# Kernel optimization log

Hardware: AMD Instinct MI355X
Metric: run time of the kernel (lower is better)

The kernel has to match this reference:

```python
import jax, jax.numpy as jnp
import numpy as np

N = 100_000
E = 1_600_000
D_IN = 128
D_OUT = 128
LN_EPS = 1e-5


def mean_agg(x, src, dst, deg):
    # out[dst] += x[src]; out /= deg  (scatter-mean over incoming edges)
    summed = jax.ops.segment_sum(x[src], dst, num_segments=N)
    return summed / deg[:, None]


def setup_inputs() -> dict:
    key = jax.random.key(0)
    ks = jax.random.split(key, 8)
    h = jax.random.normal(ks[0], (N, D_IN), dtype=jnp.float32)
    edge_index_mp = jax.random.randint(ks[1], (2, E), 0, N, dtype=jnp.int64)
    # deg = in-degree of each node (count of edges with dst == i), clamped to >= 1
    deg_mp = jax.ops.segment_sum(jnp.ones((E,), jnp.float32), edge_index_mp[1], num_segments=N)
    deg_mp = jnp.maximum(deg_mp, 1.0)
    scale = 1.0 / np.sqrt(D_IN)
    W_self = jax.random.uniform(ks[2], (D_OUT, D_IN), jnp.float32, -scale, scale)
    W_nb1 = jax.random.uniform(ks[3], (D_OUT, D_IN), jnp.float32, -scale, scale)
    W_hp = jax.random.uniform(ks[4], (D_OUT, D_IN), jnp.float32, -scale, scale)
    W_nb2 = jax.random.uniform(ks[5], (D_OUT, D_IN), jnp.float32, -scale, scale)
    bias = jnp.zeros((D_OUT,), jnp.float32)
    branch_logits = jnp.zeros((4,), jnp.float32)
    ln_gamma = jnp.ones((D_OUT,), jnp.float32)
    ln_beta = jnp.zeros((D_OUT,), jnp.float32)
    return {
        "h": h, "edge_index_mp": edge_index_mp, "deg_mp": deg_mp,
        "W_self": W_self, "W_nb1": W_nb1, "W_hp": W_hp, "W_nb2": W_nb2,
        "bias": bias, "branch_logits": branch_logits,
        "ln_gamma": ln_gamma, "ln_beta": ln_beta,
    }


def reference(h, edge_index_mp, deg_mp, W_self, W_nb1, W_hp, W_nb2,
              bias, branch_logits, ln_gamma, ln_beta):
    src, dst = edge_index_mp[0], edge_index_mp[1]
    nb1 = mean_agg(h, src, dst, deg_mp)          # 1-hop mean
    nb2 = mean_agg(nb1, src, dst, deg_mp)        # 2-hop mean
    hp = h - nb1                                  # high-pass branch
    scales = 2.0 * jax.nn.sigmoid(branch_logits)
    z = (scales[0] * (h @ W_self.T)
         + scales[1] * (nb1 @ W_nb1.T)
         + scales[2] * (hp @ W_hp.T)
         + scales[3] * (nb2 @ W_nb2.T)
         + bias)
    mu = jnp.mean(z, axis=-1, keepdims=True)
    var = jnp.var(z, axis=-1, keepdims=True)
    return (z - mu) * jax.lax.rsqrt(var + LN_EPS) * ln_gamma + ln_beta
```

## Files before the change

### kernel.cpp

```cpp
#include <hip/hip_runtime.h>

#define NN 100000
#define NE 1600000
#define D 128
#define KTOT 384
#define LN_EPS 1e-5f

#define PITCH_US 200
#define PITCH_DW 100
#define GM 64

#define SCAN_CHUNK 2048
#define NSB 49

#define NBK 196
#define BCAP 10240

#define WS_OFF_OFF   0
#define WS_OFF_CUR   401408
#define WS_OFF_BSUM  802816
#define WS_OFF_GCUR  803072
#define WS_OFF_WCBF  804096
#define WS_OFF_ESRC  967680
#define WS_OFF_GBUF  7768064
#define WS_OFF_H16   7768064
#define WS_OFF_NB1   33368064

typedef __attribute__((ext_vector_type(8))) _Float16 f16x8;
typedef __attribute__((ext_vector_type(2))) _Float16 f16x2;
typedef __attribute__((ext_vector_type(4))) float f32x4;

__device__ __forceinline__ unsigned short f2h(float f) {
    _Float16 h = (_Float16)f;
    unsigned short s; __builtin_memcpy(&s, &h, 2); return s;
}
__device__ __forceinline__ f16x2 u2h2(unsigned u) {
    f16x2 h; __builtin_memcpy(&h, &u, 4); return h;
}

__global__ void k_prep(const float* __restrict__ h, unsigned int* __restrict__ h16) {
    int i = blockIdx.x * blockDim.x + threadIdx.x;
    float2 v = reinterpret_cast<const float2*>(h)[i];
    h16[i] = (unsigned)f2h(v.x) | ((unsigned)f2h(v.y) << 16);
}

__global__ __launch_bounds__(256) void k_scan1(const float* __restrict__ deg,
                                               int* __restrict__ off,
                                               int* __restrict__ bsum) {
    __shared__ int lds[256];
    int t = threadIdx.x, b = blockIdx.x;
    int base = b * SCAN_CHUNK + t * 8;
    int v[8];
    if (base < NN) {
        float4 a0 = reinterpret_cast<const float4*>(deg + base)[0];
        float4 a1 = reinterpret_cast<const float4*>(deg + base)[1];
        v[0] = __float2int_rn(a0.x); v[1] = __float2int_rn(a0.y);
        v[2] = __float2int_rn(a0.z); v[3] = __float2int_rn(a0.w);
        v[4] = __float2int_rn(a1.x); v[5] = __float2int_rn(a1.y);
        v[6] = __float2int_rn(a1.z); v[7] = __float2int_rn(a1.w);
    } else {
        #pragma unroll
        for (int j = 0; j < 8; ++j) v[j] = 0;
    }
    int s = 0;
    #pragma unroll
    for (int j = 0; j < 8; ++j) s += v[j];
    lds[t] = s;
    __syncthreads();
    for (int ofs = 1; ofs < 256; ofs <<= 1) {
        int x = (t >= ofs) ? lds[t - ofs] : 0;
        __syncthreads();
        lds[t] += x;
        __syncthreads();
    }
    int excl = (t == 0) ? 0 : lds[t - 1];
    #pragma unroll
    for (int j = 0; j < 8; ++j) { off[base + j] = excl; excl += v[j]; }
    if (t == 255) bsum[b] = lds[255];
}

__global__ void k_scan2(int* __restrict__ bsum) {
    int t = threadIdx.x;
    int v = (t < NSB) ? bsum[t] : 0;
    #pragma unroll
    for (int ofs = 1; ofs < 64; ofs <<= 1) {
        int x = __shfl_up(v, ofs, 64);
        if (t >= ofs) v += x;
    }
    int excl = __shfl_up(v, 1, 64);
    if (t == 0) excl = 0;
    if (t < NSB) bsum[t] = excl;
    if (t == NSB - 1) bsum[NSB] = v;
}

__global__ void k_scan3(int* __restrict__ off, const int* __restrict__ bsum) {
    int i = blockIdx.x * blockDim.x + threadIdx.x;
    if (i < NN) off[i] += bsum[i >> 11];
    if (i == 0) off[NN] = bsum[NSB];
}

__global__ __launch_bounds__(256) void k_bin(const int* __restrict__ src,
                                             const int* __restrict__ dst,
                                             int* __restrict__ gcur,
                                             int2* __restrict__ gbuf) {
    __shared__ int bcnt[NBK];
    __shared__ int bbase[NBK];
    int t = threadIdx.x;
    if (t < NBK) bcnt[t] = 0;
    __syncthreads();
    int e0 = blockIdx.x * 2048;
    int s[8], d[8], r[8];
    #pragma unroll
    for (int it = 0; it < 8; ++it) {
        int e = e0 + it * 256 + t;
        bool ok = e < NE;
        s[it] = ok ? src[e] : 0;
        d[it] = ok ? dst[e] : -1;
        r[it] = ok ? atomicAdd(&bcnt[d[it] >> 9], 1) : 0;
    }
    __syncthreads();
    if (t < NBK) bbase[t] = atomicAdd(&gcur[t], bcnt[t]);
    __syncthreads();
    #pragma unroll
    for (int it = 0; it < 8; ++it) {
        if (d[it] >= 0) {
            int bk = d[it] >> 9;
            gbuf[(size_t)bk * BCAP + bbase[bk] + r[it]] = make_int2(s[it], d[it]);
        }
    }
}

__global__ __launch_bounds__(1024) void k_scatter2(const int2* __restrict__ gbuf,
                                                   const int* __restrict__ gcur,
                                                   const int* __restrict__ off,
                                                   int* __restrict__ cur,
                                                   int* __restrict__ esrc) {
    int b = blockIdx.x;
    int nb = gcur[b];
    const int2* bb = gbuf + (size_t)b * BCAP;
    for (int i = threadIdx.x; i < nb; i += 1024) {
        int2 e = bb[i];
        int p = off[e.y] + atomicAdd(&cur[e.y], 1);
        esrc[p] = e.x;
    }
}

__global__ void k_weights(const float* __restrict__ Ws, const float* __restrict__ W1,
                          const float* __restrict__ Whp, const float* __restrict__ W2,
                          const float* __restrict__ logits, unsigned short* __restrict__ wcbf) {
    int idx = blockIdx.x * blockDim.x + threadIdx.x;
    if (idx >= D * D) return;
    int o = idx >> 7, k = idx & 127;
    float s0 = 2.f / (1.f + __expf(-logits[0]));
    float s1 = 2.f / (1.f + __expf(-logits[1]));
    float s2 = 2.f / (1.f + __expf(-logits[2]));
    float s3 = 2.f / (1.f + __expf(-logits[3]));
    unsigned short b1 = f2h(s0 * Ws[idx] + s2 * Whp[idx]);
    unsigned short b2 = f2h(s1 * W1[idx] - s2 * Whp[idx]);
    unsigned short b3 = f2h(s3 * W2[idx]);
    size_t base = (size_t)o * KTOT + k;
    wcbf[base]       = b1;
    wcbf[base + 128] = b2;
    wcbf[base + 256] = b3;
}

template <bool INTERLEAVED>
__global__ __launch_bounds__(256) void k_hop(const unsigned int* __restrict__ in,
                                             unsigned int* __restrict__ outp,
                                             const int* __restrict__ off,
                                             const int* __restrict__ cnt_arr,
                                             const int* __restrict__ esrc,
                                             const float* __restrict__ deg) {
    int w = (blockIdx.x * blockDim.x + threadIdx.x) >> 6;
    int lane = threadIdx.x & 63;
    int beg = __builtin_amdgcn_readfirstlane(off[w]);
    int cnt = __builtin_amdgcn_readfirstlane(cnt_arr[w]);
    float ax = 0.f, ay = 0.f;
    for (int bs = 0; bs < cnt; bs += 64) {
        int m = cnt - bs; if (m > 64) m = 64;
        int ev = esrc[beg + bs + (lane < m ? lane : 0)];
        for (int j = 0; j < m; j += 16) {
            unsigned u[16];
            #pragma unroll
            for (int k = 0; k < 16; ++k) {
                int idx = j + k;
                int s = __builtin_amdgcn_readlane(ev, idx < m ? idx : 0);
                u[k] = in[(size_t)s * 64 + lane];
            }
            #pragma unroll
            for (int k = 0; k < 16; ++k) {
                if (j + k >= m) u[k] = 0u;
                f16x2 v = u2h2(u[k]);
                ax += (float)v.x; ay += (float)v.y;
            }
        }
    }
    float inv = 1.0f / deg[w];
    ax *= inv; ay *= inv;
    unsigned pk = (unsigned)f2h(ax) | ((unsigned)f2h(ay) << 16);
    if (INTERLEAVED) outp[(size_t)w * 128 + 64 + lane] = pk;
    else             outp[(size_t)w * 64 + lane] = pk;
}

__global__ __launch_bounds__(256) void k_gemm_ln(
    const unsigned int* __restrict__ h16,
    const unsigned int* __restrict__ nb1u,
    const unsigned short* __restrict__ wcbf, const float* __restrict__ bias,
    const float* __restrict__ gamma, const float* __restrict__ beta,
    float* __restrict__ out) {
    __shared__ __align__(16) unsigned short Xs[GM * PITCH_US];
    __shared__ float part_s[4][GM];
    __shared__ float part_q[4][GM];
    __shared__ float mu_s[GM], rs_s[GM];
    unsigned int* Xs_u = reinterpret_cast<unsigned int*>(Xs);
    const uint2* h16v = reinterpret_cast<const uint2*>(h16);
    const uint2* nb1v = reinterpret_cast<const uint2*>(nb1u);
    const uint2* outv = reinterpret_cast<const uint2*>(out);

    const int t = threadIdx.x;
    const int wv = t >> 6, lane = t & 63;
    const int lm = lane & 15, quad = lane >> 4;
    const int node0 = blockIdx.x * GM;
    const int obase = wv * 32;

    f32x4 acc[4][2] = {};

    #pragma unroll
    for (int it = 0; it < 8; ++it) {
        int i = t + 256 * it;
        int row = i >> 5, dp = i & 31;
        int rn = node0 + row; rn = rn < NN ? rn : NN - 1;
        uint2 v = h16v[(size_t)rn * 32 + dp];
        *reinterpret_cast<uint2*>(&Xs_u[row * PITCH_DW + dp * 2]) = v;
    }
    #pragma unroll
    for (int it = 0; it < 4; ++it) {
        int i = t + 256 * it;
        int row = i >> 4, dp = i & 15;
        int rn = node0 + row; rn = rn < NN ? rn : NN - 1;
        uint2 v = nb1v[(size_t)rn * 32 + dp];
        *reinterpret_cast<uint2*>(&Xs_u[row * PITCH_DW + 64 + dp * 2]) = v;
    }
    __syncthreads();

    uint2 pre1[4], pre2[8];
    #pragma unroll
    for (int it = 0; it < 4; ++it) {
        int i = t + 256 * it;
        int row = i >> 4, dp = i & 15;
        int rn = node0 + row; rn = rn < NN ? rn : NN - 1;
        pre1[it] = nb1v[(size_t)rn * 32 + 16 + dp];
    }
    #pragma unroll
    for (int it = 0; it < 8; ++it) {
        int i = t + 256 * it;
        int row = i >> 5, dp = i & 31;
        int rn = node0 + row; rn = rn < NN ? rn : NN - 1;
        pre2[it] = outv[(size_t)rn * 64 + 32 + dp];
    }

    {
        f16x8 bfr[2][6];
        #pragma unroll
        for (int nt = 0; nt < 2; ++nt) {
            const unsigned short* wp =
                wcbf + (size_t)(obase + nt * 16 + lm) * KTOT + quad * 8;
            #pragma unroll
            for (int s = 0; s < 6; ++s)
                bfr[nt][s] = *reinterpret_cast<const f16x8*>(wp + s * 32);
        }
        #pragma unroll
        for (int s = 0; s < 6; ++s) {
            int koff = s * 32 + quad * 8;
            f16x8 a[4];
            #pragma unroll
            for (int mt = 0; mt < 4; ++mt)
                a[mt] = *reinterpret_cast<const f16x8*>(&Xs[(mt * 16 + lm) * PITCH_US + koff]);
            #pragma unroll
            for (int mt = 0; mt < 4; ++mt) {
                acc[mt][0] = __builtin_amdgcn_mfma_f32_16x16x32_f16(a[mt], bfr[0][s], acc[mt][0], 0, 0, 0);
                acc[mt][1] = __builtin_amdgcn_mfma_f32_16x16x32_f16(a[mt], bfr[1][s], acc[mt][1], 0, 0, 0);
            }
        }
    }
    __syncthreads();

    #pragma unroll
    for (int it = 0; it < 4; ++it) {
        int i = t + 256 * it;
        int row = i >> 4, dp = i & 15;
        *reinterpret_cast<uint2*>(&Xs_u[row * PITCH_DW + dp * 2]) = pre1[it];
    }
    #pragma unroll
    for (int it = 0; it < 8; ++it) {
        int i = t + 256 * it;
        int row = i >> 5, dp = i & 31;
        *reinterpret_cast<uint2*>(&Xs_u[row * PITCH_DW + 32 + dp * 2]) = pre2[it];
    }
    __syncthreads();

    {
        f16x8 bfr[2][6];
        #pragma unroll
        for (int nt = 0; nt < 2; ++nt) {
            const unsigned short* wp =
                wcbf + (size_t)(obase + nt * 16 + lm) * KTOT + 192 + quad * 8;
            #pragma unroll
            for (int s = 0; s < 6; ++s)
                bfr[nt][s] = *reinterpret_cast<const f16x8*>(wp + s * 32);
        }
        #pragma unroll
        for (int s = 0; s < 6; ++s) {
            int koff = s * 32 + quad * 8;
            f16x8 a[4];
            #pragma unroll
            for (int mt = 0; mt < 4; ++mt)
                a[mt] = *reinterpret_cast<const f16x8*>(&Xs[(mt * 16 + lm) * PITCH_US + koff]);
            #pragma unroll
            for (int mt = 0; mt < 4; ++mt) {
                acc[mt][0] = __builtin_amdgcn_mfma_f32_16x16x32_f16(a[mt], bfr[0][s], acc[mt][0], 0, 0, 0);
                acc[mt][1] = __builtin_amdgcn_mfma_f32_16x16x32_f16(a[mt], bfr[1][s], acc[mt][1], 0, 0, 0);
            }
        }
    }

    float bv0 = bias[obase + lm], bv1 = bias[obase + 16 + lm];
    #pragma unroll
    for (int mt = 0; mt < 4; ++mt) {
        float s[4], q[4];
        #pragma unroll
        for (int r = 0; r < 4; ++r) {
            float v0 = acc[mt][0][r] + bv0;
            float v1 = acc[mt][1][r] + bv1;
            acc[mt][0][r] = v0;  acc[mt][1][r] = v1;
            s[r] = v0 + v1;
            q[r] = v0 * v0 + v1 * v1;
        }
        #pragma unroll
        for (int off = 1; off < 16; off <<= 1) {
            #pragma unroll
            for (int r = 0; r < 4; ++r) {
                s[r] += __shfl_xor(s[r], off, 64);
                q[r] += __shfl_xor(q[r], off, 64);
            }
        }
        if (lm == 0) {
            #pragma unroll
            for (int r = 0; r < 4; ++r) {
                part_s[wv][mt * 16 + quad * 4 + r] = s[r];
                part_q[wv][mt * 16 + quad * 4 + r] = q[r];
            }
        }
    }
    __syncthreads();
    if (t < GM) {
        float s = part_s[0][t] + part_s[1][t] + part_s[2][t] + part_s[3][t];
        float q = part_q[0][t] + part_q[1][t] + part_q[2][t] + part_q[3][t];
        float m = s * (1.f / 128.f);
        float var = q * (1.f / 128.f) - m * m;
        mu_s[t] = m;
        rs_s[t] = rsqrtf(var + LN_EPS);
    }
    __syncthreads();

    float g0 = gamma[obase + lm], g1 = gamma[obase + 16 + lm];
    float e0 = beta[obase + lm],  e1 = beta[obase + 16 + lm];
    #pragma unroll
    for (int mt = 0; mt < 4; ++mt) {
        #pragma unroll
        for (int r = 0; r < 4; ++r) {
            int lrow = mt * 16 + quad * 4 + r;
            if (node0 + lrow < NN) {
                float mu = mu_s[lrow], rs = rs_s[lrow];
                size_t ro = (size_t)(node0 + lrow) * D;
                out[ro + obase + lm]      = (acc[mt][0][r] - mu) * rs * g0 + e0;
                out[ro + obase + 16 + lm] = (acc[mt][1][r] - mu) * rs * g1 + e1;
            }
        }
    }
}

extern "C" void kernel_launch(void* const* d_in, const int* in_sizes, int n_in,
                              void* d_out, int out_size, void* d_ws, size_t ws_size,
                              hipStream_t stream) {
    const float* h      = (const float*)d_in[0];
    const int*   ei     = (const int*)d_in[1];
    const float* deg    = (const float*)d_in[2];
    const float* Wself  = (const float*)d_in[3];
    const float* Wnb1   = (const float*)d_in[4];
    const float* Whp    = (const float*)d_in[5];
    const float* Wnb2   = (const float*)d_in[6];
    const float* bias   = (const float*)d_in[7];
    const float* logits = (const float*)d_in[8];
    const float* gamma  = (const float*)d_in[9];
    const float* beta   = (const float*)d_in[10];
    float* out = (float*)d_out;

    char* ws = (char*)d_ws;
    int* off                 = (int*)(ws + WS_OFF_OFF);
    int* cur                 = (int*)(ws + WS_OFF_CUR);
    int* bsum                = (int*)(ws + WS_OFF_BSUM);
    int* gcur                = (int*)(ws + WS_OFF_GCUR);
    unsigned short* wcbf     = (unsigned short*)(ws + WS_OFF_WCBF);
    int* esrc                = (int*)(ws + WS_OFF_ESRC);
    int2* gbuf               = (int2*)(ws + WS_OFF_GBUF);
    unsigned int* h16        = (unsigned int*)(ws + WS_OFF_H16);
    unsigned int* nb1u       = (unsigned int*)(ws + WS_OFF_NB1);

    const int* src = ei;
    const int* dst = ei + NE;

    hipMemsetAsync(cur, 0, NN * sizeof(int), stream);
    hipMemsetAsync(gcur, 0, NBK * sizeof(int), stream);

    k_weights<<<64, 256, 0, stream>>>(Wself, Wnb1, Whp, Wnb2, logits, wcbf);
    k_scan1<<<NSB, 256, 0, stream>>>(deg, off, bsum);
    k_scan2<<<1, 64, 0, stream>>>(bsum);
    k_scan3<<<(NN + 255) / 256, 256, 0, stream>>>(off, bsum);
    k_bin<<<(NE + 2047) / 2048, 256, 0, stream>>>(src, dst, gcur, gbuf);
    k_scatter2<<<NBK, 1024, 0, stream>>>(gbuf, gcur, off, cur, esrc);

    k_prep<<<25000, 256, 0, stream>>>(h, h16);

    k_hop<false><<<(NN * 64) / 256, 256, 0, stream>>>(h16, nb1u, off, cur, esrc, deg);
    k_hop<true><<<(NN * 64) / 256, 256, 0, stream>>>(nb1u, (unsigned int*)out, off, cur, esrc, deg);

    k_gemm_ln<<<(NN + GM - 1) / GM, 256, 0, stream>>>(h16, nb1u, wcbf, bias, gamma, beta, out);
}
```

Before: 350.4 us.

## Fuse scan, weight prep, edge binning and fp16 conversion into one front kernel

Merges k_scan1, k_weights, k_bin and k_prep into a single k_front launch whose block ranges are dispatched by block index. The cur array is now zeroed inside the scan blocks instead of by a separate memset, and the fp16 conversion of h now does 16 floats per thread with wide stores. The bin buffer gbuf is moved to alias the nb1 region rather than h16, because h16 is now written concurrently with binning. This removes several launches and their gaps and lets independent preprocessing phases overlap, at the cost of one kernel with mixed register and LDS use and reliance on workspace aliasing staying correct.

```diff
diff --git a/kernel.cpp b/kernel.cpp
--- a/kernel.cpp
+++ b/kernel.cpp
@@ -15,6 +15,12 @@
 
 #define NBK 196
 #define BCAP 10240
+
+#define FB_SCAN1   0
+#define FB_WEIGHTS 49
+#define FB_BIN     113
+#define FB_PREP    895
+#define FB_TOTAL   4020
 
 #define WS_OFF_OFF   0
 #define WS_OFF_CUR   401408
@@ -22,9 +28,9 @@
 #define WS_OFF_GCUR  803072
 #define WS_OFF_WCBF  804096
 #define WS_OFF_ESRC  967680
-#define WS_OFF_GBUF  7768064
 #define WS_OFF_H16   7768064
 #define WS_OFF_NB1   33368064
+#define WS_OFF_GBUF  33368064
 
 typedef __attribute__((ext_vector_type(8))) _Float16 f16x8;
 typedef __attribute__((ext_vector_type(2))) _Float16 f16x2;
@@ -37,46 +43,105 @@
 __device__ __forceinline__ f16x2 u2h2(unsigned u) {
     f16x2 h; __builtin_memcpy(&h, &u, 4); return h;
 }
-
-__global__ void k_prep(const float* __restrict__ h, unsigned int* __restrict__ h16) {
-    int i = blockIdx.x * blockDim.x + threadIdx.x;
-    float2 v = reinterpret_cast<const float2*>(h)[i];
-    h16[i] = (unsigned)f2h(v.x) | ((unsigned)f2h(v.y) << 16);
-}
-
-__global__ __launch_bounds__(256) void k_scan1(const float* __restrict__ deg,
-                                               int* __restrict__ off,
-                                               int* __restrict__ bsum) {
+__device__ __forceinline__ unsigned pk2(float a, float b) {
+    return (unsigned)f2h(a) | ((unsigned)f2h(b) << 16);
+}
+
+__global__ __launch_bounds__(256) void k_front(
+    const float* __restrict__ deg, int* __restrict__ off, int* __restrict__ bsum,
+    int* __restrict__ cur,
+    const float* __restrict__ Ws, const float* __restrict__ W1,
+    const float* __restrict__ Whp, const float* __restrict__ W2,
+    const float* __restrict__ logits, unsigned short* __restrict__ wcbf,
+    const int* __restrict__ src, const int* __restrict__ dst,
+    int* __restrict__ gcur, int2* __restrict__ gbuf,
+    const float* __restrict__ h, unsigned int* __restrict__ h16) {
     __shared__ int lds[256];
-    int t = threadIdx.x, b = blockIdx.x;
-    int base = b * SCAN_CHUNK + t * 8;
-    int v[8];
-    if (base < NN) {
-        float4 a0 = reinterpret_cast<const float4*>(deg + base)[0];
-        float4 a1 = reinterpret_cast<const float4*>(deg + base)[1];
-        v[0] = __float2int_rn(a0.x); v[1] = __float2int_rn(a0.y);
-        v[2] = __float2int_rn(a0.z); v[3] = __float2int_rn(a0.w);
-        v[4] = __float2int_rn(a1.x); v[5] = __float2int_rn(a1.y);
-        v[6] = __float2int_rn(a1.z); v[7] = __float2int_rn(a1.w);
+    __shared__ int bcnt[NBK];
+    __shared__ int bbase[NBK];
+    const int b = blockIdx.x;
+    const int t = threadIdx.x;
+
+    if (b < FB_WEIGHTS) {
+        int base = b * SCAN_CHUNK + t * 8;
+        *reinterpret_cast<int4*>(cur + base) = make_int4(0, 0, 0, 0);
+        *reinterpret_cast<int4*>(cur + base + 4) = make_int4(0, 0, 0, 0);
+        int v[8];
+        if (base < NN) {
+            float4 a0 = reinterpret_cast<const float4*>(deg + base)[0];
+            float4 a1 = reinterpret_cast<const float4*>(deg + base)[1];
+            v[0] = __float2int_rn(a0.x); v[1] = __float2int_rn(a0.y);
+            v[2] = __float2int_rn(a0.z); v[3] = __float2int_rn(a0.w);
+            v[4] = __float2int_rn(a1.x); v[5] = __float2int_rn(a1.y);
+            v[6] = __float2int_rn(a1.z); v[7] = __float2int_rn(a1.w);
+        } else {
+            #pragma unroll
+            for (int j = 0; j < 8; ++j) v[j] = 0;
+        }
+        int s = 0;
+        #pragma unroll
+        for (int j = 0; j < 8; ++j) s += v[j];
+        lds[t] = s;
+        __syncthreads();
+        for (int ofs = 1; ofs < 256; ofs <<= 1) {
+            int x = (t >= ofs) ? lds[t - ofs] : 0;
+            __syncthreads();
+            lds[t] += x;
+            __syncthreads();
+        }
+        int excl = (t == 0) ? 0 : lds[t - 1];
+        #pragma unroll
+        for (int j = 0; j < 8; ++j) { off[base + j] = excl; excl += v[j]; }
+        if (t == 255) bsum[b] = lds[255];
+    } else if (b < FB_BIN) {
+        int idx = (b - FB_WEIGHTS) * 256 + t;
+        int o = idx >> 7, k = idx & 127;
+        float s0 = 2.f / (1.f + __expf(-logits[0]));
+        float s1 = 2.f / (1.f + __expf(-logits[1]));
+        float s2 = 2.f / (1.f + __expf(-logits[2]));
+        float s3 = 2.f / (1.f + __expf(-logits[3]));
+        unsigned short b1 = f2h(s0 * Ws[idx] + s2 * Whp[idx]);
+        unsigned short b2 = f2h(s1 * W1[idx] - s2 * Whp[idx]);
+        unsigned short b3 = f2h(s3 * W2[idx]);
+        size_t base = (size_t)o * KTOT + k;
+        wcbf[base]       = b1;
+        wcbf[base + 128] = b2;
+        wcbf[base + 256] = b3;
+    } else if (b < FB_PREP) {
+        if (t < NBK) bcnt[t] = 0;
+        __syncthreads();
+        int e0 = (b - FB_BIN) * 2048;
+        int s[8], d[8], r[8];
+        #pragma unroll
+        for (int it = 0; it < 8; ++it) {
+            int e = e0 + it * 256 + t;
+            bool ok = e < NE;
+            s[it] = ok ? src[e] : 0;
+            d[it] = ok ? dst[e] : -1;
+            r[it] = ok ? atomicAdd(&bcnt[d[it] >> 9], 1) : 0;
+        }
+        __syncthreads();
+        if (t < NBK) bbase[t] = atomicAdd(&gcur[t], bcnt[t]);
+        __syncthreads();
+        #pragma unroll
+        for (int it = 0; it < 8; ++it) {
+            if (d[it] >= 0) {
+                int bk = d[it] >> 9;
+                gbuf[(size_t)bk * BCAP + bbase[bk] + r[it]] = make_int2(s[it], d[it]);
+            }
+        }
     } else {
-        #pragma unroll
-        for (int j = 0; j < 8; ++j) v[j] = 0;
-    }
-    int s = 0;
-    #pragma unroll
-    for (int j = 0; j < 8; ++j) s += v[j];
-    lds[t] = s;
-    __syncthreads();
-    for (int ofs = 1; ofs < 256; ofs <<= 1) {
-        int x = (t >= ofs) ? lds[t - ofs] : 0;
-        __syncthreads();
-        lds[t] += x;
-        __syncthreads();
-    }
-    int excl = (t == 0) ? 0 : lds[t - 1];
-    #pragma unroll
-    for (int j = 0; j < 8; ++j) { off[base + j] = excl; excl += v[j]; }
-    if (t == 255) bsum[b] = lds[255];
+        int g2 = (b - FB_PREP) * 256 + t;
+        const float4* hv = reinterpret_cast<const float4*>(h) + (size_t)g2 * 4;
+        float4 a = hv[0], bb = hv[1], c = hv[2], dd = hv[3];
+        uint4 o0, o1;
+        o0.x = pk2(a.x, a.y);   o0.y = pk2(a.z, a.w);
+        o0.z = pk2(bb.x, bb.y); o0.w = pk2(bb.z, bb.w);
+        o1.x = pk2(c.x, c.y);   o1.y = pk2(c.z, c.w);
+        o1.z = pk2(dd.x, dd.y); o1.w = pk2(dd.z, dd.w);
+        reinterpret_cast<uint4*>(h16)[(size_t)g2 * 2]     = o0;
+        reinterpret_cast<uint4*>(h16)[(size_t)g2 * 2 + 1] = o1;
+    }
 }
 
 __global__ void k_scan2(int* __restrict__ bsum) {
@@ -97,37 +162,6 @@
     int i = blockIdx.x * blockDim.x + threadIdx.x;
     if (i < NN) off[i] += bsum[i >> 11];
     if (i == 0) off[NN] = bsum[NSB];
-}
-
-__global__ __launch_bounds__(256) void k_bin(const int* __restrict__ src,
-                                             const int* __restrict__ dst,
-                                             int* __restrict__ gcur,
-                                             int2* __restrict__ gbuf) {
-    __shared__ int bcnt[NBK];
-    __shared__ int bbase[NBK];
-    int t = threadIdx.x;
-    if (t < NBK) bcnt[t] = 0;
-    __syncthreads();
-    int e0 = blockIdx.x * 2048;
-    int s[8], d[8], r[8];
-    #pragma unroll
-    for (int it = 0; it < 8; ++it) {
-        int e = e0 + it * 256 + t;
-        bool ok = e < NE;
-        s[it] = ok ? src[e] : 0;
-        d[it] = ok ? dst[e] : -1;
-        r[it] = ok ? atomicAdd(&bcnt[d[it] >> 9], 1) : 0;
-    }
-    __syncthreads();
-    if (t < NBK) bbase[t] = atomicAdd(&gcur[t], bcnt[t]);
-    __syncthreads();
-    #pragma unroll
-    for (int it = 0; it < 8; ++it) {
-        if (d[it] >= 0) {
-            int bk = d[it] >> 9;
-            gbuf[(size_t)bk * BCAP + bbase[bk] + r[it]] = make_int2(s[it], d[it]);
-        }
-    }
 }
 
 __global__ __launch_bounds__(1024) void k_scatter2(const int2* __restrict__ gbuf,
@@ -143,25 +177,6 @@
         int p = off[e.y] + atomicAdd(&cur[e.y], 1);
         esrc[p] = e.x;
     }
-}
-
-__global__ void k_weights(const float* __restrict__ Ws, const float* __restrict__ W1,
-                          const float* __restrict__ Whp, const float* __restrict__ W2,
-                          const float* __restrict__ logits, unsigned short* __restrict__ wcbf) {
-    int idx = blockIdx.x * blockDim.x + threadIdx.x;
-    if (idx >= D * D) return;
-    int o = idx >> 7, k = idx & 127;
-    float s0 = 2.f / (1.f + __expf(-logits[0]));
-    float s1 = 2.f / (1.f + __expf(-logits[1]));
-    float s2 = 2.f / (1.f + __expf(-logits[2]));
-    float s3 = 2.f / (1.f + __expf(-logits[3]));
-    unsigned short b1 = f2h(s0 * Ws[idx] + s2 * Whp[idx]);
-    unsigned short b2 = f2h(s1 * W1[idx] - s2 * Whp[idx]);
-    unsigned short b3 = f2h(s3 * W2[idx]);
-    size_t base = (size_t)o * KTOT + k;
-    wcbf[base]       = b1;
-    wcbf[base + 128] = b2;
-    wcbf[base + 256] = b3;
 }
 
 template <bool INTERLEAVED>
@@ -410,17 +425,14 @@
     const int* src = ei;
     const int* dst = ei + NE;
 
-    hipMemsetAsync(cur, 0, NN * sizeof(int), stream);
     hipMemsetAsync(gcur, 0, NBK * sizeof(int), stream);
 
-    k_weights<<<64, 256, 0, stream>>>(Wself, Wnb1, Whp, Wnb2, logits, wcbf);
-    k_scan1<<<NSB, 256, 0, stream>>>(deg, off, bsum);
+    k_front<<<FB_TOTAL, 256, 0, stream>>>(deg, off, bsum, cur,
+                                          Wself, Wnb1, Whp, Wnb2, logits, wcbf,
+                                          src, dst, gcur, gbuf, h, h16);
     k_scan2<<<1, 64, 0, stream>>>(bsum);
     k_scan3<<<(NN + 255) / 256, 256, 0, stream>>>(off, bsum);
-    k_bin<<<(NE + 2047) / 2048, 256, 0, stream>>>(src, dst, gcur, gbuf);
     k_scatter2<<<NBK, 1024, 0, stream>>>(gbuf, gcur, off, cur, esrc);
-
-    k_prep<<<25000, 256, 0, stream>>>(h, h16);
 
     k_hop<false><<<(NN * 64) / 256, 256, 0, stream>>>(h16, nb1u, off, cur, esrc, deg);
     k_hop<true><<<(NN * 64) / 256, 256, 0, stream>>>(nb1u, (unsigned int*)out, off, cur, esrc, deg);
```

New measurement: 330.8 us. 5.6% less time.
